# Performance work log

Measured on AMD Instinct MI355X. Metric: run time of the kernel, lower is better.

## Reference

```python
import jax, jax.numpy as jnp
import numpy as np

B, N, DIM = 8, 8192, 512
H, DH = 8, 64
INNER = H * DH
EPS = 1e-5


def setup_inputs() -> dict:
    key = jax.random.key(0)
    ks = jax.random.split(key, 5)
    x = jax.random.normal(ks[0], (B, N, DIM), dtype=jnp.float32)
    w_qkv = jax.random.normal(ks[1], (DIM, 3 * INNER), dtype=jnp.float32) * (DIM ** -0.5)
    ln_w = jnp.ones((INNER,), dtype=jnp.float32)
    ln_b = jnp.zeros((INNER,), dtype=jnp.float32)
    w_out = jax.random.normal(ks[2], (INNER, DIM), dtype=jnp.float32) * (INNER ** -0.5)
    b_out = jnp.zeros((DIM,), dtype=jnp.float32)
    return {"x": x, "w_qkv": w_qkv, "ln_w": ln_w, "ln_b": ln_b,
            "w_out": w_out, "b_out": b_out}


def _layernorm(x, w, b):
    mu = jnp.mean(x, axis=-1, keepdims=True)
    var = jnp.mean(jnp.square(x - mu), axis=-1, keepdims=True)
    return (x - mu) * jax.lax.rsqrt(var + EPS) * w + b


def reference(x, w_qkv, ln_w, ln_b, w_out, b_out):
    b, n, _ = x.shape
    qkv = x @ w_qkv  # [b, n, 3*inner]
    q, k, v = jnp.split(qkv, 3, axis=-1)
    # b n (h d) -> b h n d
    def heads(t):
        return t.reshape(b, n, H, DH).transpose(0, 2, 1, 3)
    q, k, v = heads(q), heads(k), heads(v)
    q = jax.nn.relu(q)
    k = jax.nn.relu(k)
    kv = jnp.einsum('bhnm,bhnd->bhmd', k, v)   # [b, h, d, d]
    out = jnp.einsum('bhnm,bhmd->bhnd', q, kv)  # [b, h, n, d]
    out = out.transpose(0, 2, 1, 3).reshape(b, n, INNER)
    out = _layernorm(out, ln_w, ln_b)
    return out @ w_out + b_out
```

## Files before the change

kernel.cpp:

```cpp
#include <hip/hip_runtime.h>
#include <stdint.h>

#define B_ 8
#define N_ 8192
#define DIM_ 512
#define H_ 8
#define DH_ 64
#define ROWS (B_*N_)
#define TRIPLE (3*DIM_)
#define EPS_ 1e-5f

typedef __attribute__((ext_vector_type(8))) short short8;
typedef __attribute__((ext_vector_type(4))) float f32x4;
typedef __attribute__((ext_vector_type(4))) float fl4;
typedef __attribute__((ext_vector_type(4))) unsigned short us4;
typedef __attribute__((ext_vector_type(8))) unsigned short us8;

#define AS1 __attribute__((address_space(1)))
#define AS3 __attribute__((address_space(3)))

__device__ __forceinline__ void gld16(const void* g, void* l) {
    __builtin_amdgcn_global_load_lds((const AS1 void*)(uintptr_t)g,
                                     (AS3 void*)(unsigned)(uintptr_t)l, 16, 0, 0);
}

__device__ inline unsigned short f2bf(float f) {
    union { float f; unsigned int u; } x; x.f = f;
    unsigned int r = x.u + 0x7fffu + ((x.u >> 16) & 1u);
    return (unsigned short)(r >> 16);
}
__device__ inline float bf2f(unsigned short b) {
    union { unsigned int u; float f; } x; x.u = ((unsigned int)b) << 16;
    return x.f;
}

__device__ __forceinline__ int eoff(int row, int col) {
    return row * 64 + (col ^ ((((unsigned)row >> 2) & 3) << 4));
}

__global__ __launch_bounds__(256) void k_cvt(const float* __restrict__ x,
                                             unsigned short* __restrict__ xb) {
    size_t i = ((size_t)blockIdx.x * 256 + threadIdx.x) * 8;
    fl4 a = *(const fl4*)(x + i);
    fl4 b = *(const fl4*)(x + i + 4);
    us8 r;
    r[0] = f2bf(a[0]); r[1] = f2bf(a[1]); r[2] = f2bf(a[2]); r[3] = f2bf(a[3]);
    r[4] = f2bf(b[0]); r[5] = f2bf(b[1]); r[6] = f2bf(b[2]); r[7] = f2bf(b[3]);
    *(us8*)(xb + i) = r;
}

__global__ __launch_bounds__(256) void k_prep(const float* __restrict__ wq,
        const float* __restrict__ wo,
        unsigned short* __restrict__ wqT, unsigned short* __restrict__ woT) {
    __shared__ float T[32][33];
    int bid = blockIdx.x;
    const float* src; unsigned short* dst; int srcCols, dstCols, k0, n0;
    if (bid < 768) {
        int tn = bid % 48, tk = bid / 48;
        src = wq; dst = wqT; srcCols = 1536; dstCols = 512;
        k0 = tk * 32; n0 = tn * 32;
    } else {
        int b = bid - 768;
        int tn = b % 16, tk = b / 16;
        src = wo; dst = woT; srcCols = 512; dstCols = 512;
        k0 = tk * 32; n0 = tn * 32;
    }
    int t = threadIdx.x, r = t >> 3, c4 = (t & 7) * 4;
    fl4 v = *(const fl4*)(src + (size_t)(k0 + r) * srcCols + n0 + c4);
    T[c4 + 0][r] = v[0]; T[c4 + 1][r] = v[1];
    T[c4 + 2][r] = v[2]; T[c4 + 3][r] = v[3];
    __syncthreads();
    us4 o;
    o[0] = f2bf(T[r][c4 + 0]); o[1] = f2bf(T[r][c4 + 1]);
    o[2] = f2bf(T[r][c4 + 2]); o[3] = f2bf(T[r][c4 + 3]);
    *(us4*)(dst + (size_t)(n0 + r) * dstCols + k0 + c4) = o;
}

__global__ __launch_bounds__(512, 4) void k_qkv8(const unsigned short* __restrict__ xb,
        const unsigned short* __restrict__ wT,
        unsigned short* __restrict__ qkv)
{
    __shared__ __align__(1024) unsigned short LDSb[3][12288];

    const int tid  = threadIdx.x;
    const int lane = tid & 63;
    const int wid  = tid >> 6;
    const int wr   = wid >> 1;
    const int wc   = wid & 1;
    const int lr   = lane & 15;

    int id  = blockIdx.x;
    int nid = (id & 7) * 384 + (id >> 3);
    int n0  = (nid % 12) * 128;
    int m0  = (nid / 12) * 256;

    const unsigned short* pA[2];
    const unsigned short* pB1;
    unsigned ldstA[2], ldstB;
#pragma unroll
    for (int j = 0; j < 2; ++j) {
        int s    = tid + j * 512;
        int row  = ((s >> 6) << 4) + ((s >> 2) & 15);
        int colb = ((s & 3) << 4) ^ (((s >> 5) & 1) << 5);
        pA[j] = xb + (size_t)(m0 + row) * 512 + (colb >> 1);
        ldstA[j] = (unsigned)((j * 512 + wid * 64) * 8);
    }
    {
        int s    = tid;
        int row  = ((s >> 6) << 4) + ((s >> 2) & 15);
        int colb = ((s & 3) << 4) ^ (((s >> 5) & 1) << 5);
        pB1 = wT + (size_t)(n0 + row) * 512 + (colb >> 1);
        ldstB = (unsigned)(8192 + wid * 64 * 8);
    }
    const int kg = (lane >> 4) * 8;
    const int lo = lr * 32 + (kg ^ ((lr >> 3) << 4));

    auto STAGE = [&](int t, int slot) {
        gld16(pA[0] + t * 32, (void*)&LDSb[slot][ldstA[0]]);
        gld16(pA[1] + t * 32, (void*)&LDSb[slot][ldstA[1]]);
        gld16(pB1   + t * 32, (void*)&LDSb[slot][ldstB]);
    };

    f32x4 acc[4][4] = {};
    short8 af[4], bfr[4];

    STAGE(0, 0);
    STAGE(1, 1);

#define WAITV(n) asm volatile("s_waitcnt vmcnt(" #n ")" ::: "memory")
#pragma unroll
    for (int t = 0; t < 16; ++t) {
        if (t <= 14) WAITV(3);
        else         WAITV(0);
        __builtin_amdgcn_s_barrier();
        __builtin_amdgcn_sched_barrier(0);

        if (t + 2 < 16) STAGE(t + 2, (t + 2) % 3);

        const unsigned short* L = LDSb[t % 3];
#pragma unroll
        for (int m = 0; m < 4; ++m)
            af[m] = *(const short8*)&L[(wr * 4 + m) * 512 + lo];
#pragma unroll
        for (int n = 0; n < 4; ++n)
            bfr[n] = *(const short8*)&L[8192 + (wc * 4 + n) * 512 + lo];

        __builtin_amdgcn_s_setprio(1);
#pragma unroll
        for (int m = 0; m < 4; ++m)
#pragma unroll
            for (int n = 0; n < 4; ++n)
                acc[m][n] = __builtin_amdgcn_mfma_f32_16x16x32_bf16(af[m], bfr[n], acc[m][n], 0, 0, 0);
        __builtin_amdgcn_s_setprio(0);
    }
#undef WAITV

    __syncthreads();

    unsigned short* S = ((unsigned short*)LDSb) + wid * 4096;
    const bool relu_tile = (n0 < 1024);
#pragma unroll
    for (int m = 0; m < 4; ++m) {
        int rbase = m * 16 + ((lane >> 4) << 2);
#pragma unroll
        for (int n = 0; n < 4; ++n) {
            int col = n * 16 + lr;
#pragma unroll
            for (int r = 0; r < 4; ++r) {
                float v = acc[m][n][r];
                if (relu_tile && v < 0.0f) v = 0.0f;
                S[eoff(rbase + r, col)] = f2bf(v);
            }
        }
    }
    __syncthreads();
    {
        int rsub = lane >> 3, sub = lane & 7;
        size_t grow = (size_t)(m0 + wr * 64);
        int gcol = n0 + wc * 64 + sub * 8;
#pragma unroll
        for (int rd = 0; rd < 8; ++rd) {
            int row = rd * 8 + rsub;
            short8 vv = *(const short8*)&S[eoff(row, sub * 8)];
            *(short8*)(qkv + (grow + row) * TRIPLE + gcol) = vv;
        }
    }
}

__global__ __launch_bounds__(256) void k_qkv_f(const float* __restrict__ x,
        const unsigned short* __restrict__ wT,
        unsigned short* __restrict__ qkv)
{
    __shared__ unsigned short As[128][40];
    __shared__ unsigned short Bs[128][40];
    int t = threadIdx.x;
    int lane = t & 63, wave = t >> 6;
    int m0 = blockIdx.y * 128;
    int n0 = blockIdx.x * 128;
    int wm = (wave & 1) * 64, wn = (wave >> 1) * 64;
    int lr = lane & 15, kg = (lane >> 4) * 8;

    f32x4 acc[4][4] = {};
    for (int k0 = 0; k0 < DIM_; k0 += 32) {
#pragma unroll
        for (int i = 0; i < 4; ++i) {
            int c = t + 256 * i;
            int r = c >> 3, c4 = (c & 7) * 4;
            fl4 v = *(const fl4*)(x + (size_t)(m0 + r) * DIM_ + k0 + c4);
            unsigned short* dst = &As[r][c4];
            dst[0] = f2bf(v[0]); dst[1] = f2bf(v[1]); dst[2] = f2bf(v[2]); dst[3] = f2bf(v[3]);
        }
#pragma unroll
        for (int i = 0; i < 2; ++i) {
            int c = t + 256 * i;
            int r = c >> 2, c8 = (c & 3) * 8;
            *(int4*)&Bs[r][c8] = *(const int4*)(wT + (size_t)(n0 + r) * DIM_ + k0 + c8);
        }
        __syncthreads();
        short8 af[4], bfr[4];
#pragma unroll
        for (int i = 0; i < 4; ++i) af[i]  = *(short8*)&As[wm + i*16 + lr][kg];
#pragma unroll
        for (int j = 0; j < 4; ++j) bfr[j] = *(short8*)&Bs[wn + j*16 + lr][kg];
#pragma unroll
        for (int i = 0; i < 4; ++i)
#pragma unroll
            for (int j = 0; j < 4; ++j)
                acc[i][j] = __builtin_amdgcn_mfma_f32_16x16x32_bf16(af[i], bfr[j], acc[i][j], 0, 0, 0);
        __syncthreads();
    }
#pragma unroll
    for (int i = 0; i < 4; ++i) {
        int row = m0 + wm + i*16 + (lane >> 4) * 4;
#pragma unroll
        for (int j = 0; j < 4; ++j) {
            int col = n0 + wn + j*16 + (lane & 15);
            bool rl = (col < 1024);
#pragma unroll
            for (int r = 0; r < 4; ++r) {
                float v = acc[i][j][r];
                if (rl && v < 0.0f) v = 0.0f;
                qkv[(size_t)(row + r) * TRIPLE + col] = f2bf(v);
            }
        }
    }
}

__global__ __launch_bounds__(256) void k_kv(const unsigned short* __restrict__ qkv,
                                            float* __restrict__ kv)
{
    __shared__ unsigned short KT[64][136];
    __shared__ unsigned short VT[64][136];
    __shared__ float red[64 * 64];
    int t = threadIdx.x, lane = t & 63, wave = t >> 6;
    int bh = blockIdx.x;
    int b = bh >> 3, h = bh & 7;
    int chunk = blockIdx.y;
    size_t rowbase = (size_t)b * N_ + (size_t)chunk * 1024;
    int kcol = DIM_ + h * 64;
    int vcol = 2 * DIM_ + h * 64;
    int lr = lane & 15;

    f32x4 acc[4][4] = {};
    for (int tile = 0; tile < 8; ++tile) {
        size_t r0 = rowbase + tile * 128;
#pragma unroll
        for (int i = 0; i < 2; ++i) {
            int u = t + 256 * i;
            int rp = u >> 3;
            int c8 = (u & 7) * 8;
            size_t ra = r0 + 2 * rp, rb = ra + 1;
            us8 ka = *(const us8*)(qkv + ra * TRIPLE + kcol + c8);
            us8 kb = *(const us8*)(qkv + rb * TRIPLE + kcol + c8);
            us8 va = *(const us8*)(qkv + ra * TRIPLE + vcol + c8);
            us8 vb = *(const us8*)(qkv + rb * TRIPLE + vcol + c8);
#pragma unroll
            for (int j = 0; j < 8; ++j) {
                int d = c8 + j;
                *(unsigned int*)&KT[d][2 * rp] =
                    (unsigned int)ka[j] | ((unsigned int)kb[j] << 16);
                *(unsigned int*)&VT[d][2 * rp] =
                    (unsigned int)va[j] | ((unsigned int)vb[j] << 16);
            }
        }
        __syncthreads();
        int kg = wave * 32 + (lane >> 4) * 8;
        short8 af[4], bfr[4];
#pragma unroll
        for (int i = 0; i < 4; ++i) af[i]  = *(short8*)&KT[i*16 + lr][kg];
#pragma unroll
        for (int j = 0; j < 4; ++j) bfr[j] = *(short8*)&VT[j*16 + lr][kg];
#pragma unroll
        for (int i = 0; i < 4; ++i)
#pragma unroll
            for (int j = 0; j < 4; ++j)
                acc[i][j] = __builtin_amdgcn_mfma_f32_16x16x32_bf16(af[i], bfr[j], acc[i][j], 0, 0, 0);
        __syncthreads();
    }
    for (int w = 0; w < 4; ++w) {
        if (wave == w) {
#pragma unroll
            for (int i = 0; i < 4; ++i)
#pragma unroll
                for (int j = 0; j < 4; ++j)
#pragma unroll
                    for (int r = 0; r < 4; ++r) {
                        int m = i*16 + (lane >> 4) * 4 + r;
                        int d = j*16 + (lane & 15);
                        if (w == 0) red[m * 64 + d] = acc[i][j][r];
                        else        red[m * 64 + d] += acc[i][j][r];
                    }
        }
        __syncthreads();
    }
    float* kvout = kv + (size_t)bh * 4096;
#pragma unroll
    for (int i = 0; i < 16; ++i) {
        int idx = t + 256 * i;
        atomicAdd(&kvout[idx], red[idx]);
    }
}

__global__ __launch_bounds__(256) void k_attn(unsigned short* __restrict__ qkv,
                                              const float* __restrict__ kv,
                                              float* __restrict__ rowstats)
{
    __shared__ unsigned short Qh[128][72];
    __shared__ unsigned short kvT[64][72];
    __shared__ __align__(64) unsigned short Sout[128 * 64];
    int t = threadIdx.x, lane = t & 63, wave = t >> 6;
    size_t r0 = (size_t)blockIdx.x * 128;
    int b = (int)(r0 / N_);
    int lr = lane & 15;

    float s8[8] = {}, ss8[8] = {};

    for (int h = 0; h < H_; ++h) {
#pragma unroll
        for (int i = 0; i < 4; ++i) {
            int c = t + 256 * i;
            int r = c >> 3, f8 = (c & 7) * 8;
            *(us8*)&Qh[r][f8] = *(const us8*)(qkv + (r0 + r) * TRIPLE + h * 64 + f8);
        }
        const float* kvh = kv + (size_t)(b * 8 + h) * 4096;
#pragma unroll
        for (int i = 0; i < 16; ++i) {
            int idx = t + 256 * i;
            int m = idx >> 6, d = idx & 63;
            kvT[d][m] = f2bf(kvh[idx]);
        }
        __syncthreads();
        f32x4 acc[2][4] = {};
#pragma unroll
        for (int ks = 0; ks < 2; ++ks) {
            int kg = ks * 32 + (lane >> 4) * 8;
            short8 af[2], bfr[4];
#pragma unroll
            for (int i = 0; i < 2; ++i) af[i]  = *(short8*)&Qh[wave*32 + i*16 + lr][kg];
#pragma unroll
            for (int j = 0; j < 4; ++j) bfr[j] = *(short8*)&kvT[j*16 + lr][kg];
#pragma unroll
            for (int i = 0; i < 2; ++i)
#pragma unroll
                for (int j = 0; j < 4; ++j)
                    acc[i][j] = __builtin_amdgcn_mfma_f32_16x16x32_bf16(af[i], bfr[j], acc[i][j], 0, 0, 0);
        }
#pragma unroll
        for (int i = 0; i < 2; ++i)
#pragma unroll
            for (int j = 0; j < 4; ++j) {
                int rbase = wave*32 + i*16 + (lane >> 4) * 4;
                int col = j*16 + lr;
#pragma unroll
                for (int r = 0; r < 4; ++r) {
                    float v = acc[i][j][r];
                    s8[i*4+r]  += v;
                    ss8[i*4+r] += v * v;
                    Sout[eoff(rbase + r, col)] = f2bf(v);
                }
            }
        __syncthreads();
        {
            int sub = t & 7, rsub = t >> 3;
#pragma unroll
            for (int rd = 0; rd < 4; ++rd) {
                int row = rd * 32 + rsub;
                short8 vv = *(const short8*)&Sout[eoff(row, sub * 8)];
                *(short8*)(qkv + (r0 + row) * TRIPLE + h * 64 + sub * 8) = vv;
            }
        }
        __syncthreads();
    }

#pragma unroll
    for (int q = 0; q < 8; ++q) {
        float s = s8[q], ss = ss8[q];
        s += __shfl_xor(s, 1);  ss += __shfl_xor(ss, 1);
        s += __shfl_xor(s, 2);  ss += __shfl_xor(ss, 2);
        s += __shfl_xor(s, 4);  ss += __shfl_xor(ss, 4);
        s += __shfl_xor(s, 8);  ss += __shfl_xor(ss, 8);
        s8[q] = s; ss8[q] = ss;
    }
    if (lr == 0) {
#pragma unroll
        for (int q = 0; q < 8; ++q) {
            int row = wave*32 + (q >> 2)*16 + (lane >> 4)*4 + (q & 3);
            float m = s8[q] * (1.0f / 512.0f);
            float rs = rsqrtf(ss8[q] * (1.0f / 512.0f) - m * m + EPS_);
            rowstats[2 * (r0 + row)]     = m;
            rowstats[2 * (r0 + row) + 1] = rs;
        }
    }
}

__global__ __launch_bounds__(256) void k_out(const unsigned short* __restrict__ qkv,
        const unsigned short* __restrict__ woutT,
        const float* __restrict__ rowstats,
        const float* __restrict__ lnw, const float* __restrict__ lnb,
        const float* __restrict__ bout, float* __restrict__ out)
{
    __shared__ unsigned short As[128][40];
    __shared__ unsigned short Bs[128][40];
    __shared__ float mu[128], rs[128], lw[512], lb[512];
    int t = threadIdx.x, lane = t & 63, wave = t >> 6;
    int id  = blockIdx.y * 4 + blockIdx.x;
    int nid = (id & 7) * 256 + (id >> 3);
    int m0  = (nid >> 2) * 128;
    int n0  = (nid & 3) * 128;
    int wm = (wave & 1) * 64, wn = (wave >> 1) * 64;
    int lr = lane & 15, kg = (lane >> 4) * 8;

    for (int i = t; i < 512; i += 256) { lw[i] = lnw[i]; lb[i] = lnb[i]; }
    if (t < 128) {
        mu[t] = rowstats[2 * (m0 + t)];
        rs[t] = rowstats[2 * (m0 + t) + 1];
    }
    __syncthreads();

    f32x4 acc[4][4] = {};
    for (int k0 = 0; k0 < 512; k0 += 32) {
#pragma unroll
        for (int i = 0; i < 4; ++i) {
            int c = t + 256 * i;
            int r = c >> 3, c4 = (c & 7) * 4;
            us4 v = *(const us4*)(qkv + (size_t)(m0 + r) * TRIPLE + k0 + c4);
            float mm = mu[r], rr = rs[r];
            unsigned short* dst = &As[r][c4];
#pragma unroll
            for (int j = 0; j < 4; ++j) {
                float f = (bf2f(v[j]) - mm) * rr * lw[k0 + c4 + j] + lb[k0 + c4 + j];
                dst[j] = f2bf(f);
            }
        }
#pragma unroll
        for (int i = 0; i < 2; ++i) {
            int c = t + 256 * i;
            int r = c >> 2, c8 = (c & 3) * 8;
            *(int4*)&Bs[r][c8] = *(const int4*)(woutT + (size_t)(n0 + r) * DIM_ + k0 + c8);
        }
        __syncthreads();
        short8 af[4], bfr[4];
#pragma unroll
        for (int i = 0; i < 4; ++i) af[i]  = *(short8*)&As[wm + i*16 + lr][kg];
#pragma unroll
        for (int j = 0; j < 4; ++j) bfr[j] = *(short8*)&Bs[wn + j*16 + lr][kg];
#pragma unroll
        for (int i = 0; i < 4; ++i)
#pragma unroll
            for (int j = 0; j < 4; ++j)
                acc[i][j] = __builtin_amdgcn_mfma_f32_16x16x32_bf16(af[i], bfr[j], acc[i][j], 0, 0, 0);
        __syncthreads();
    }
#pragma unroll
    for (int i = 0; i < 4; ++i) {
        int row = m0 + wm + i*16 + (lane >> 4) * 4;
#pragma unroll
        for (int j = 0; j < 4; ++j) {
            int col = n0 + wn + j*16 + (lane & 15);
            float bo = bout[col];
#pragma unroll
            for (int r = 0; r < 4; ++r)
                out[(size_t)(row + r) * DIM_ + col] = acc[i][j][r] + bo;
        }
    }
}

extern "C" void kernel_launch(void* const* d_in, const int* in_sizes, int n_in,
                              void* d_out, int out_size, void* d_ws, size_t ws_size,
                              hipStream_t stream) {
    (void)in_sizes; (void)n_in; (void)out_size;
    const float* x     = (const float*)d_in[0];
    const float* w_qkv = (const float*)d_in[1];
    const float* ln_w  = (const float*)d_in[2];
    const float* ln_b  = (const float*)d_in[3];
    const float* w_out = (const float*)d_in[4];
    const float* b_out = (const float*)d_in[5];
    float* out = (float*)d_out;

    char* ws = (char*)d_ws;
    const size_t QKV_BYTES = (size_t)ROWS * TRIPLE * sizeof(unsigned short);
    const size_t KV_BYTES  = (size_t)64 * 64 * 64 * sizeof(float);
    const size_t WQT_BYTES = (size_t)TRIPLE * DIM_ * sizeof(unsigned short);
    const size_t WOT_BYTES = (size_t)DIM_ * DIM_ * sizeof(unsigned short);
    const size_t RS_BYTES  = (size_t)ROWS * 2 * sizeof(float);
    const size_t XB_BYTES  = (size_t)ROWS * DIM_ * sizeof(unsigned short);
    unsigned short* qkv   = (unsigned short*)ws;
    float*          kvbuf = (float*)(ws + QKV_BYTES);
    unsigned short* wqkvT = (unsigned short*)(ws + QKV_BYTES + KV_BYTES);
    unsigned short* woutT = (unsigned short*)(ws + QKV_BYTES + KV_BYTES + WQT_BYTES);
    float*          rstat = (float*)(ws + QKV_BYTES + KV_BYTES + WQT_BYTES + WOT_BYTES);
    unsigned short* xb    = (unsigned short*)(ws + QKV_BYTES + KV_BYTES + WQT_BYTES + WOT_BYTES + RS_BYTES);
    const size_t NEED = QKV_BYTES + KV_BYTES + WQT_BYTES + WOT_BYTES + RS_BYTES + XB_BYTES;

    hipMemsetAsync(kvbuf, 0, KV_BYTES, stream);
    k_prep<<<1024, 256, 0, stream>>>(w_qkv, w_out, wqkvT, woutT);
    if (ws_size >= NEED) {
        k_cvt<<<16384, 256, 0, stream>>>(x, xb);
        k_qkv8<<<dim3(3072), 512, 0, stream>>>(xb, wqkvT, qkv);
    } else {
        k_qkv_f<<<dim3(12, 512), 256, 0, stream>>>(x, wqkvT, qkv);
    }
    k_kv<<<dim3(64, 8), 256, 0, stream>>>(qkv, kvbuf);
    k_attn<<<512, 256, 0, stream>>>(qkv, kvbuf, rstat);
    k_out<<<dim3(4, 512), 256, 0, stream>>>(qkv, woutT, rstat, ln_w, ln_b, b_out, out);
}
```

Measured before the change: 525.5 us.

## Fuse layernorm into attention kernel and pretranspose kv to bf16

```diff
diff --git a/kernel.cpp b/kernel.cpp
--- a/kernel.cpp
+++ b/kernel.cpp
@@ -321,18 +321,43 @@
     }
 }
 
+__global__ __launch_bounds__(256) void k_kvt(const float* __restrict__ kv,
+                                             unsigned short* __restrict__ kvtb) {
+    __shared__ float T[64][65];
+    int bh = blockIdx.x, t = threadIdx.x;
+    const float* src = kv + (size_t)bh * 4096;
+    unsigned short* dst = kvtb + (size_t)bh * 4096;
+#pragma unroll
+    for (int i = 0; i < 16; ++i) {
+        int idx = t + 256 * i;
+        T[idx & 63][idx >> 6] = src[idx];
+    }
+    __syncthreads();
+#pragma unroll
+    for (int i = 0; i < 16; ++i) {
+        int idx = t + 256 * i;
+        dst[idx] = f2bf(T[idx >> 6][idx & 63]);
+    }
+}
+
 __global__ __launch_bounds__(256) void k_attn(unsigned short* __restrict__ qkv,
-                                              const float* __restrict__ kv,
-                                              float* __restrict__ rowstats)
+                                              const unsigned short* __restrict__ kvtb,
+                                              const float* __restrict__ lnw,
+                                              const float* __restrict__ lnb)
 {
     __shared__ unsigned short Qh[128][72];
     __shared__ unsigned short kvT[64][72];
     __shared__ __align__(64) unsigned short Sout[128 * 64];
+    __shared__ float muS[128], rsS[128];
     int t = threadIdx.x, lane = t & 63, wave = t >> 6;
     size_t r0 = (size_t)blockIdx.x * 128;
     int b = (int)(r0 / N_);
     int lr = lane & 15;
 
+    float lw8[8], lb8[8];
+#pragma unroll
+    for (int j = 0; j < 8; ++j) { lw8[j] = lnw[lane * 8 + j]; lb8[j] = lnb[lane * 8 + j]; }
+
     float s8[8] = {}, ss8[8] = {};
 
     for (int h = 0; h < H_; ++h) {
@@ -342,12 +367,12 @@
             int r = c >> 3, f8 = (c & 7) * 8;
             *(us8*)&Qh[r][f8] = *(const us8*)(qkv + (r0 + r) * TRIPLE + h * 64 + f8);
         }
-        const float* kvh = kv + (size_t)(b * 8 + h) * 4096;
-#pragma unroll
-        for (int i = 0; i < 16; ++i) {
-            int idx = t + 256 * i;
-            int m = idx >> 6, d = idx & 63;
-            kvT[d][m] = f2bf(kvh[idx]);
+        const unsigned short* kvh = kvtb + (size_t)(b * 8 + h) * 4096;
+#pragma unroll
+        for (int i = 0; i < 2; ++i) {
+            int c = t + 256 * i;
+            int d = c >> 3, m8 = (c & 7) * 8;
+            *(us8*)&kvT[d][m8] = *(const us8*)(kvh + d * 64 + m8);
         }
         __syncthreads();
         f32x4 acc[2][4] = {};
@@ -406,22 +431,32 @@
         for (int q = 0; q < 8; ++q) {
             int row = wave*32 + (q >> 2)*16 + (lane >> 4)*4 + (q & 3);
             float m = s8[q] * (1.0f / 512.0f);
-            float rs = rsqrtf(ss8[q] * (1.0f / 512.0f) - m * m + EPS_);
-            rowstats[2 * (r0 + row)]     = m;
-            rowstats[2 * (r0 + row) + 1] = rs;
-        }
+            muS[row] = m;
+            rsS[row] = rsqrtf(ss8[q] * (1.0f / 512.0f) - m * m + EPS_);
+        }
+    }
+    __syncthreads();
+
+#pragma unroll
+    for (int i = 0; i < 32; ++i) {
+        int row = wave + 4 * i;
+        unsigned short* p = qkv + (r0 + row) * TRIPLE + lane * 8;
+        us8 v = *(const us8*)p;
+        float mm = muS[row], rr = rsS[row];
+        us8 o;
+#pragma unroll
+        for (int j = 0; j < 8; ++j)
+            o[j] = f2bf((bf2f(v[j]) - mm) * rr * lw8[j] + lb8[j]);
+        *(us8*)p = o;
     }
 }
 
 __global__ __launch_bounds__(256) void k_out(const unsigned short* __restrict__ qkv,
         const unsigned short* __restrict__ woutT,
-        const float* __restrict__ rowstats,
-        const float* __restrict__ lnw, const float* __restrict__ lnb,
         const float* __restrict__ bout, float* __restrict__ out)
 {
     __shared__ unsigned short As[128][40];
     __shared__ unsigned short Bs[128][40];
-    __shared__ float mu[128], rs[128], lw[512], lb[512];
     int t = threadIdx.x, lane = t & 63, wave = t >> 6;
     int id  = blockIdx.y * 4 + blockIdx.x;
     int nid = (id & 7) * 256 + (id >> 3);
@@ -430,27 +465,13 @@
     int wm = (wave & 1) * 64, wn = (wave >> 1) * 64;
     int lr = lane & 15, kg = (lane >> 4) * 8;
 
-    for (int i = t; i < 512; i += 256) { lw[i] = lnw[i]; lb[i] = lnb[i]; }
-    if (t < 128) {
-        mu[t] = rowstats[2 * (m0 + t)];
-        rs[t] = rowstats[2 * (m0 + t) + 1];
-    }
-    __syncthreads();
-
     f32x4 acc[4][4] = {};
     for (int k0 = 0; k0 < 512; k0 += 32) {
 #pragma unroll
-        for (int i = 0; i < 4; ++i) {
+        for (int i = 0; i < 2; ++i) {
             int c = t + 256 * i;
-            int r = c >> 3, c4 = (c & 7) * 4;
-            us4 v = *(const us4*)(qkv + (size_t)(m0 + r) * TRIPLE + k0 + c4);
-            float mm = mu[r], rr = rs[r];
-            unsigned short* dst = &As[r][c4];
-#pragma unroll
-            for (int j = 0; j < 4; ++j) {
-                float f = (bf2f(v[j]) - mm) * rr * lw[k0 + c4 + j] + lb[k0 + c4 + j];
-                dst[j] = f2bf(f);
-            }
+            int r = c >> 2, c8 = (c & 3) * 8;
+            *(int4*)&As[r][c8] = *(const int4*)(qkv + (size_t)(m0 + r) * TRIPLE + k0 + c8);
         }
 #pragma unroll
         for (int i = 0; i < 2; ++i) {
@@ -502,15 +523,15 @@
     const size_t KV_BYTES  = (size_t)64 * 64 * 64 * sizeof(float);
     const size_t WQT_BYTES = (size_t)TRIPLE * DIM_ * sizeof(unsigned short);
     const size_t WOT_BYTES = (size_t)DIM_ * DIM_ * sizeof(unsigned short);
-    const size_t RS_BYTES  = (size_t)ROWS * 2 * sizeof(float);
+    const size_t KVT_BYTES = (size_t)64 * 64 * 64 * sizeof(unsigned short);
     const size_t XB_BYTES  = (size_t)ROWS * DIM_ * sizeof(unsigned short);
     unsigned short* qkv   = (unsigned short*)ws;
     float*          kvbuf = (float*)(ws + QKV_BYTES);
     unsigned short* wqkvT = (unsigned short*)(ws + QKV_BYTES + KV_BYTES);
     unsigned short* woutT = (unsigned short*)(ws + QKV_BYTES + KV_BYTES + WQT_BYTES);
-    float*          rstat = (float*)(ws + QKV_BYTES + KV_BYTES + WQT_BYTES + WOT_BYTES);
-    unsigned short* xb    = (unsigned short*)(ws + QKV_BYTES + KV_BYTES + WQT_BYTES + WOT_BYTES + RS_BYTES);
-    const size_t NEED = QKV_BYTES + KV_BYTES + WQT_BYTES + WOT_BYTES + RS_BYTES + XB_BYTES;
+    unsigned short* kvtb  = (unsigned short*)(ws + QKV_BYTES + KV_BYTES + WQT_BYTES + WOT_BYTES);
+    unsigned short* xb    = (unsigned short*)(ws + QKV_BYTES + KV_BYTES + WQT_BYTES + WOT_BYTES + KVT_BYTES);
+    const size_t NEED = QKV_BYTES + KV_BYTES + WQT_BYTES + WOT_BYTES + KVT_BYTES + XB_BYTES;
 
     hipMemsetAsync(kvbuf, 0, KV_BYTES, stream);
     k_prep<<<1024, 256, 0, stream>>>(w_qkv, w_out, wqkvT, woutT);
@@ -521,6 +542,7 @@
         k_qkv_f<<<dim3(12, 512), 256, 0, stream>>>(x, wqkvT, qkv);
     }
     k_kv<<<dim3(64, 8), 256, 0, stream>>>(qkv, kvbuf);
-    k_attn<<<512, 256, 0, stream>>>(qkv, kvbuf, rstat);
-    k_out<<<dim3(4, 512), 256, 0, stream>>>(qkv, woutT, rstat, ln_w, ln_b, b_out, out);
-}
+    k_kvt<<<64, 256, 0, stream>>>(kvbuf, kvtb);
+    k_attn<<<512, 256, 0, stream>>>(qkv, kvtb, ln_w, ln_b);
+    k_out<<<dim3(4, 512), 256, 0, stream>>>(qkv, woutT, b_out, out);
+}
```

New measurement: 525.8 us. No clear change (+0.1%).
